# Performance work log

Measured on AMD Instinct MI355X. Metric: run time of the kernel, lower is better.

Reference implementation:

```python
import jax, jax.numpy as jnp
import numpy as np

N_NODES = 100000
N_EDGES = 1600000
N_FEAT = 128
N_CLASSES = 10
N_GRAPHS = 256


def setup_inputs() -> dict:
    key = jax.random.key(0)
    ks = jax.random.split(key, 16)
    x = jax.random.normal(ks[0], (N_NODES, N_FEAT), dtype=jnp.float32)
    edge_index = jax.random.randint(ks[1], (2, N_EDGES), 0, N_NODES, dtype=jnp.int64)
    batch = jnp.sort(jax.random.randint(ks[2], (N_NODES,), 0, N_GRAPHS, dtype=jnp.int64))
    s = 0.1
    # GAT1: in=128 -> heads=8, out_per_head=8, concat -> 64
    W1 = jax.random.normal(ks[3], (N_FEAT, 64), dtype=jnp.float32) * s
    a_src1 = jax.random.normal(ks[4], (8, 8), dtype=jnp.float32) * s
    a_dst1 = jax.random.normal(ks[5], (8, 8), dtype=jnp.float32) * s
    b1 = jnp.zeros((64,), jnp.float32)
    # GAT2: in=64 -> heads=1, out=128
    W2 = jax.random.normal(ks[6], (64, 128), dtype=jnp.float32) * s
    a_src2 = jax.random.normal(ks[7], (1, 128), dtype=jnp.float32) * s
    a_dst2 = jax.random.normal(ks[8], (1, 128), dtype=jnp.float32) * s
    b2 = jnp.zeros((128,), jnp.float32)
    fc_w = jax.random.normal(ks[9], (128, N_CLASSES), dtype=jnp.float32) * s
    fc_b = jnp.zeros((N_CLASSES,), jnp.float32)
    return {"x": x, "edge_index": edge_index, "batch": batch,
            "W1": W1, "a_src1": a_src1, "a_dst1": a_dst1, "b1": b1,
            "W2": W2, "a_src2": a_src2, "a_dst2": a_dst2, "b2": b2,
            "fc_w": fc_w, "fc_b": fc_b}


def _segment_softmax(e, seg, n):
    # e: [E, H]; softmax over edges sharing the same destination node
    m = jax.ops.segment_max(e, seg, num_segments=n)
    m = jnp.where(jnp.isfinite(m), m, jnp.zeros_like(m))  # guard isolated nodes
    ex = jnp.exp(e - m[seg])
    s = jax.ops.segment_sum(ex, seg, num_segments=n)
    return ex / (s[seg] + jnp.asarray(1e-16, e.dtype))


def _gat_conv(x, src, dst, W, a_src, a_dst, bias):
    # PyG GATConv (eval mode, self-loops already appended to src/dst)
    H, C = a_src.shape
    n = x.shape[0]
    h = (x @ W).reshape(n, H, C)                      # [N,H,C]
    al_s = jnp.einsum('nhc,hc->nh', h, a_src)          # [N,H]
    al_d = jnp.einsum('nhc,hc->nh', h, a_dst)
    e = jax.nn.leaky_relu(al_s[src] + al_d[dst], 0.2)  # [E,H]
    alpha = _segment_softmax(e, dst, n)                # [E,H]
    out = jax.ops.segment_sum(h[src] * alpha[..., None], dst, num_segments=n)  # [N,H,C]
    return out.reshape(n, H * C) + bias                # concat=True (H=1 layer2 is identity reshape)


def reference(x, edge_index, batch, W1, a_src1, a_dst1, b1, W2, a_src2, a_dst2, b2, fc_w, fc_b):
    n = x.shape[0]
    loop = jnp.arange(n, dtype=edge_index.dtype)
    src = jnp.concatenate([edge_index[0], loop])       # add self-loops (PyG default)
    dst = jnp.concatenate([edge_index[1], loop])
    x1 = jax.nn.relu(_gat_conv(x, src, dst, W1, a_src1, a_dst1, b1))
    # dropout p=0.6 is identity in eval mode
    x2 = _gat_conv(x1, src, dst, W2, a_src2, a_dst2, b2)
    cnt = jax.ops.segment_sum(jnp.ones((n,), x2.dtype), batch, num_segments=N_GRAPHS)
    pooled = jax.ops.segment_sum(x2, batch, num_segments=N_GRAPHS) / jnp.maximum(cnt, 1.0)[:, None]
    logits = pooled @ fc_w + fc_b
    return jax.nn.log_softmax(logits, axis=1)
```

## Files before the change

### kernel.cpp

```cpp
#include <hip/hip_runtime.h>
#include <math.h>

typedef unsigned int uint;
typedef unsigned short ushort;
typedef unsigned char uchar;
typedef __attribute__((ext_vector_type(2))) float v2f;

#define S1 4.0f
#define S2 16.0f

template <bool HI>
__device__ inline v2f fp8x2f(uint u) {
    return __builtin_amdgcn_cvt_pk_f32_fp8((int)u, HI);
}

__global__ __launch_bounds__(256) void k_gemm1(const float* __restrict__ x,
                                               const float* __restrict__ W1,
                                               const float* __restrict__ as1,
                                               const float* __restrict__ ad1,
                                               uchar* __restrict__ h1f8,
                                               float* __restrict__ al1s,
                                               float* __restrict__ al1d, int N) {
    __shared__ float sB[128 * 64];
    __shared__ float sA[64 * 68];
    const int t = threadIdx.x;
    const int n0 = blockIdx.x * 64;
    {
        const float4* w4 = (const float4*)W1;
        float4* s4 = (float4*)sB;
#pragma unroll
        for (int i = 0; i < 8; ++i) s4[t + i * 256] = w4[t + i * 256];
    }
    const int r0 = (t >> 3) * 2;
    const int c0 = (t & 7) * 8;
    float acc0[8] = {0, 0, 0, 0, 0, 0, 0, 0};
    float acc1[8] = {0, 0, 0, 0, 0, 0, 0, 0};
    for (int kb = 0; kb < 2; ++kb) {
        __syncthreads();
#pragma unroll
        for (int i = 0; i < 4; ++i) {
            int idx = t + i * 256;
            int r = idx >> 4, kc = idx & 15;
            int n = n0 + r;
            float4 v = make_float4(0.f, 0.f, 0.f, 0.f);
            if (n < N) v = ((const float4*)x)[(size_t)n * 32 + kb * 16 + kc];
            *(float4*)&sA[r * 68 + kc * 4] = v;
        }
        __syncthreads();
        const float* bptr = &sB[kb * 64 * 64];
#pragma unroll 8
        for (int kk = 0; kk < 64; ++kk) {
            float a0 = sA[r0 * 68 + kk];
            float a1 = sA[(r0 + 1) * 68 + kk];
            const float* bp = &bptr[kk * 64 + c0];
            float4 b0 = *(const float4*)bp;
            float4 b1v = *(const float4*)(bp + 4);
            acc0[0] += a0 * b0.x; acc0[1] += a0 * b0.y; acc0[2] += a0 * b0.z; acc0[3] += a0 * b0.w;
            acc0[4] += a0 * b1v.x; acc0[5] += a0 * b1v.y; acc0[6] += a0 * b1v.z; acc0[7] += a0 * b1v.w;
            acc1[0] += a1 * b0.x; acc1[1] += a1 * b0.y; acc1[2] += a1 * b0.z; acc1[3] += a1 * b0.w;
            acc1[4] += a1 * b1v.x; acc1[5] += a1 * b1v.y; acc1[6] += a1 * b1v.z; acc1[7] += a1 * b1v.w;
        }
    }
    float ps0 = 0.f, pd0 = 0.f, ps1 = 0.f, pd1 = 0.f;
#pragma unroll
    for (int i = 0; i < 8; ++i) {
        float ws = as1[c0 + i], wd = ad1[c0 + i];
        ps0 += acc0[i] * ws; pd0 += acc0[i] * wd;
        ps1 += acc1[i] * ws; pd1 += acc1[i] * wd;
    }
    int n = n0 + r0;
    int head = t & 7;
    if (n < N) {
        int q0 = 0, q1 = 0;
        q0 = __builtin_amdgcn_cvt_pk_fp8_f32(acc0[0] * S1, acc0[1] * S1, q0, false);
        q0 = __builtin_amdgcn_cvt_pk_fp8_f32(acc0[2] * S1, acc0[3] * S1, q0, true);
        q1 = __builtin_amdgcn_cvt_pk_fp8_f32(acc0[4] * S1, acc0[5] * S1, q1, false);
        q1 = __builtin_amdgcn_cvt_pk_fp8_f32(acc0[6] * S1, acc0[7] * S1, q1, true);
        uint2 p; p.x = (uint)q0; p.y = (uint)q1;
        *(uint2*)&h1f8[(size_t)n * 64 + c0] = p;
        al1s[(size_t)n * 8 + head] = ps0;
        al1d[(size_t)n * 8 + head] = pd0;
    }
    if (n + 1 < N) {
        int q0 = 0, q1 = 0;
        q0 = __builtin_amdgcn_cvt_pk_fp8_f32(acc1[0] * S1, acc1[1] * S1, q0, false);
        q0 = __builtin_amdgcn_cvt_pk_fp8_f32(acc1[2] * S1, acc1[3] * S1, q0, true);
        q1 = __builtin_amdgcn_cvt_pk_fp8_f32(acc1[4] * S1, acc1[5] * S1, q1, false);
        q1 = __builtin_amdgcn_cvt_pk_fp8_f32(acc1[6] * S1, acc1[7] * S1, q1, true);
        uint2 p; p.x = (uint)q0; p.y = (uint)q1;
        *(uint2*)&h1f8[(size_t)(n + 1) * 64 + c0] = p;
        al1s[(size_t)(n + 1) * 8 + head] = ps1;
        al1d[(size_t)(n + 1) * 8 + head] = pd1;
    }
}

__global__ __launch_bounds__(256) void k_gemm2(const float* __restrict__ x1pre,
                                               const float* __restrict__ W2,
                                               const float* __restrict__ b1,
                                               const float* __restrict__ as2,
                                               const float* __restrict__ ad2,
                                               uchar* __restrict__ h2f8,
                                               float* __restrict__ al2s,
                                               float* __restrict__ al2d, int N) {
    __shared__ float sB[64 * 128];
    __shared__ float sA[64 * 68];
    const int t = threadIdx.x;
    const int n0 = blockIdx.x * 64;
    {
        const float4* w4 = (const float4*)W2;
        float4* s4 = (float4*)sB;
#pragma unroll
        for (int i = 0; i < 8; ++i) s4[t + i * 256] = w4[t + i * 256];
    }
#pragma unroll
    for (int i = 0; i < 4; ++i) {
        int idx = t + i * 256;
        int r = idx >> 4, kc = idx & 15;
        int n = n0 + r;
        float4 v = make_float4(0.f, 0.f, 0.f, 0.f);
        if (n < N) {
            v = ((const float4*)x1pre)[(size_t)n * 16 + kc];
            float4 bb = ((const float4*)b1)[kc];
            v.x = fmaxf(v.x + bb.x, 0.f);
            v.y = fmaxf(v.y + bb.y, 0.f);
            v.z = fmaxf(v.z + bb.z, 0.f);
            v.w = fmaxf(v.w + bb.w, 0.f);
        }
        *(float4*)&sA[r * 68 + kc * 4] = v;
    }
    __syncthreads();
    const int r0 = (t >> 3) * 2;
    const int cb = (t & 7) * 4;
    float acc0[16], acc1[16];
#pragma unroll
    for (int i = 0; i < 16; ++i) { acc0[i] = 0.f; acc1[i] = 0.f; }
#pragma unroll 4
    for (int k = 0; k < 64; ++k) {
        float a0 = sA[r0 * 68 + k];
        float a1 = sA[(r0 + 1) * 68 + k];
#pragma unroll
        for (int j = 0; j < 4; ++j) {
            float4 b = *(const float4*)&sB[k * 128 + cb + 32 * j];
            acc0[j * 4 + 0] += a0 * b.x; acc0[j * 4 + 1] += a0 * b.y;
            acc0[j * 4 + 2] += a0 * b.z; acc0[j * 4 + 3] += a0 * b.w;
            acc1[j * 4 + 0] += a1 * b.x; acc1[j * 4 + 1] += a1 * b.y;
            acc1[j * 4 + 2] += a1 * b.z; acc1[j * 4 + 3] += a1 * b.w;
        }
    }
    float ps0 = 0.f, pd0 = 0.f, ps1 = 0.f, pd1 = 0.f;
#pragma unroll
    for (int j = 0; j < 4; ++j)
#pragma unroll
        for (int i = 0; i < 4; ++i) {
            int cc = cb + 32 * j + i;
            float ws = as2[cc], wd = ad2[cc];
            ps0 += acc0[j * 4 + i] * ws; pd0 += acc0[j * 4 + i] * wd;
            ps1 += acc1[j * 4 + i] * ws; pd1 += acc1[j * 4 + i] * wd;
        }
#pragma unroll
    for (int off = 1; off < 8; off <<= 1) {
        ps0 += __shfl_xor(ps0, off); pd0 += __shfl_xor(pd0, off);
        ps1 += __shfl_xor(ps1, off); pd1 += __shfl_xor(pd1, off);
    }
    int n = n0 + r0;
    if (n < N) {
#pragma unroll
        for (int j = 0; j < 4; ++j) {
            int q = 0;
            q = __builtin_amdgcn_cvt_pk_fp8_f32(acc0[j * 4 + 0] * S2, acc0[j * 4 + 1] * S2, q, false);
            q = __builtin_amdgcn_cvt_pk_fp8_f32(acc0[j * 4 + 2] * S2, acc0[j * 4 + 3] * S2, q, true);
            *(uint*)&h2f8[(size_t)n * 128 + cb + 32 * j] = (uint)q;
        }
        if ((t & 7) == 0) { al2s[n] = ps0; al2d[n] = pd0; }
    }
    if (n + 1 < N) {
#pragma unroll
        for (int j = 0; j < 4; ++j) {
            int q = 0;
            q = __builtin_amdgcn_cvt_pk_fp8_f32(acc1[j * 4 + 0] * S2, acc1[j * 4 + 1] * S2, q, false);
            q = __builtin_amdgcn_cvt_pk_fp8_f32(acc1[j * 4 + 2] * S2, acc1[j * 4 + 3] * S2, q, true);
            *(uint*)&h2f8[(size_t)(n + 1) * 128 + cb + 32 * j] = (uint)q;
        }
        if ((t & 7) == 0) { al2s[n + 1] = ps1; al2d[n + 1] = pd1; }
    }
}


__global__ __launch_bounds__(256) void k_hist(const int* __restrict__ dst,
                                              int* __restrict__ counts,
                                              int E, int CH, int NB) {
    __shared__ int hist[784];
    int t = threadIdx.x, b = blockIdx.x;
    for (int k = t; k < NB; k += 256) hist[k] = 0;
    __syncthreads();
    int e0 = b * CH;
    int e1 = e0 + CH; if (e1 > E) e1 = E;
    for (int e = e0 + t; e < e1; e += 256)
        atomicAdd(&hist[dst[e] >> 7], 1);
    __syncthreads();
    for (int k = t; k < NB; k += 256) counts[(size_t)b * NB + k] = hist[k];
}

__global__ __launch_bounds__(256) void k_bscan(int* __restrict__ counts,
                                               int* __restrict__ btot,
                                               int C, int NB) {
    __shared__ int sh[256];
    int t = threadIdx.x, k = blockIdx.x;
    int v[4];
#pragma unroll
    for (int i = 0; i < 4; ++i) {
        int b = t * 4 + i;
        v[i] = (b < C) ? counts[(size_t)b * NB + k] : 0;
    }
    int s = v[0] + v[1] + v[2] + v[3];
    sh[t] = s;
    __syncthreads();
    int accv = s;
    for (int off = 1; off < 256; off <<= 1) {
        int u = (t >= off) ? sh[t - off] : 0;
        __syncthreads();
        accv += u;
        sh[t] = accv;
        __syncthreads();
    }
    int excl = accv - s;
#pragma unroll
    for (int i = 0; i < 4; ++i) {
        int b = t * 4 + i;
        if (b < C) counts[(size_t)b * NB + k] = excl;
        excl += v[i];
    }
    if (t == 255) btot[k] = accv;
}

__global__ void k_bscan2(const int* __restrict__ btot, int* __restrict__ bbase,
                         int NB, int E) {
    __shared__ int sh[1024];
    int t = threadIdx.x;
    int v = (t < NB) ? btot[t] : 0;
    sh[t] = v;
    __syncthreads();
    int accv = v;
    for (int off = 1; off < 1024; off <<= 1) {
        int u = (t >= off) ? sh[t - off] : 0;
        __syncthreads();
        accv += u;
        sh[t] = accv;
        __syncthreads();
    }
    if (t < NB) bbase[t] = accv - v;
    if (t == 0) bbase[NB] = E;
}

__global__ __launch_bounds__(256) void k_bucket(const int* __restrict__ src,
                                                const int* __restrict__ dst,
                                                const int* __restrict__ counts,
                                                const int* __restrict__ bbase,
                                                int2* __restrict__ ebuf,
                                                int E, int CH, int NB) {
    __shared__ int pos[784];
    int t = threadIdx.x, b = blockIdx.x;
    for (int k = t; k < NB; k += 256)
        pos[k] = bbase[k] + counts[(size_t)b * NB + k];
    __syncthreads();
    int e0 = b * CH;
    int e1 = e0 + CH; if (e1 > E) e1 = E;
    for (int e = e0 + t; e < e1; e += 256) {
        int d = dst[e], s = src[e];
        int p = atomicAdd(&pos[d >> 7], 1);
        ebuf[p] = make_int2(s, d);
    }
}

__global__ __launch_bounds__(256) void k_csr(const int* __restrict__ bbase,
                                             const int2* __restrict__ ebuf,
                                             int* __restrict__ row_ptr,
                                             int* __restrict__ col,
                                             int N, int E) {
    __shared__ int cnt[128];
    __shared__ int fill[128];
    __shared__ int rowb[128];
    __shared__ int sh[256];
    int t = threadIdx.x, k = blockIdx.x;
    int lo = bbase[k], hi = bbase[k + 1];
    int nlo = k << 7;
    int nn = N - nlo; if (nn > 128) nn = 128;
    if (t < 128) { cnt[t] = 0; fill[t] = 0; }
    __syncthreads();
    for (int i = lo + t; i < hi; i += 256)
        atomicAdd(&cnt[ebuf[i].y & 127], 1);
    __syncthreads();
    int v = (t < nn) ? (cnt[t] + 1) : 0;
    sh[t] = v;
    __syncthreads();
    int accv = v;
    for (int off = 1; off < 256; off <<= 1) {
        int u = (t >= off) ? sh[t - off] : 0;
        __syncthreads();
        accv += u;
        sh[t] = accv;
        __syncthreads();
    }
    int fbase = lo + nlo;
    if (t < nn) {
        int rb = fbase + accv - v;
        rowb[t] = rb;
        row_ptr[nlo + t] = rb;
        col[rb + cnt[t]] = nlo + t;
    }
    if (k == 0 && t == 0) row_ptr[N] = E + N;
    __syncthreads();
    for (int i = lo + t; i < hi; i += 256) {
        int2 e = ebuf[i];
        int j = e.y & 127;
        int r = atomicAdd(&fill[j], 1);
        col[rowb[j] + r] = e.x;
    }
}

__global__ __launch_bounds__(256) void k_edge1(const uchar* __restrict__ h1f8,
                                               const float* __restrict__ al1s,
                                               const float* __restrict__ al1d,
                                               const int* __restrict__ row_ptr,
                                               const int* __restrict__ col,
                                               float* __restrict__ x1pre, int N) {
    int node = blockIdx.x * 4 + (threadIdx.x >> 6);
    if (node >= N) return;
    const int lane = threadIdx.x & 63;
    const int e8 = lane >> 3;
    const int h = lane & 7;
    const int g = lane >> 4;
    const int k4 = lane & 15;
    const int hh = k4 >> 1;
    float a_d = al1d[(size_t)node * 8 + h];
    const int s0 = row_ptr[node], s1 = row_ptr[node + 1];
    float den_part = 0.f;
    float acc[4] = {0.f, 0.f, 0.f, 0.f};
    for (int base = s0; base < s1; base += 64) {
        int idx = base + lane;
        int cidx = idx < s1 ? idx : s1 - 1;
        int my_col = col[cidx];
        int cnt = s1 - base; if (cnt > 64) cnt = 64;
        int cntR = (cnt + 7) & ~7;
        int i = 0;
        for (; i + 16 <= cntR; i += 16) {
            int cA = __shfl(my_col, i + g);
            int cB = __shfl(my_col, i + 4 + g);
            int cC = __shfl(my_col, i + 8 + g);
            int cD = __shfl(my_col, i + 12 + g);
            uint hA = *(const uint*)(h1f8 + (size_t)cA * 64 + k4 * 4);
            uint hB = *(const uint*)(h1f8 + (size_t)cB * 64 + k4 * 4);
            uint hC = *(const uint*)(h1f8 + (size_t)cC * 64 + k4 * 4);
            uint hD = *(const uint*)(h1f8 + (size_t)cD * 64 + k4 * 4);
            int c0 = __shfl(my_col, i + e8);
            int c1 = __shfl(my_col, i + 8 + e8);
            float e0v = al1s[(size_t)c0 * 8 + h] + a_d;
            float e1v = al1s[(size_t)c1 * 8 + h] + a_d;
            e0v = e0v > 0.f ? e0v : 0.2f * e0v;
            e1v = e1v > 0.f ? e1v : 0.2f * e1v;
            float w0 = (base + i + e8 < s1) ? __expf(e0v) : 0.f;
            float w1 = (base + i + 8 + e8 < s1) ? __expf(e1v) : 0.f;
            den_part += w0 + w1;
            float wA = __shfl(w0, g * 8 + hh);
            float wB = __shfl(w0, (4 + g) * 8 + hh);
            float wC = __shfl(w1, g * 8 + hh);
            float wD = __shfl(w1, (4 + g) * 8 + hh);
            v2f p;
            p = fp8x2f<false>(hA); acc[0] += wA * p.x; acc[1] += wA * p.y;
            p = fp8x2f<true>(hA);  acc[2] += wA * p.x; acc[3] += wA * p.y;
            p = fp8x2f<false>(hB); acc[0] += wB * p.x; acc[1] += wB * p.y;
            p = fp8x2f<true>(hB);  acc[2] += wB * p.x; acc[3] += wB * p.y;
            p = fp8x2f<false>(hC); acc[0] += wC * p.x; acc[1] += wC * p.y;
            p = fp8x2f<true>(hC);  acc[2] += wC * p.x; acc[3] += wC * p.y;
            p = fp8x2f<false>(hD); acc[0] += wD * p.x; acc[1] += wD * p.y;
            p = fp8x2f<true>(hD);  acc[2] += wD * p.x; acc[3] += wD * p.y;
        }
        if (i < cntR) {
            int cA = __shfl(my_col, i + g);
            int cB = __shfl(my_col, i + 4 + g);
            uint hA = *(const uint*)(h1f8 + (size_t)cA * 64 + k4 * 4);
            uint hB = *(const uint*)(h1f8 + (size_t)cB * 64 + k4 * 4);
            int c0 = __shfl(my_col, i + e8);
            float e0v = al1s[(size_t)c0 * 8 + h] + a_d;
            e0v = e0v > 0.f ? e0v : 0.2f * e0v;
            float w0 = (base + i + e8 < s1) ? __expf(e0v) : 0.f;
            den_part += w0;
            float wA = __shfl(w0, g * 8 + hh);
            float wB = __shfl(w0, (4 + g) * 8 + hh);
            v2f p;
            p = fp8x2f<false>(hA); acc[0] += wA * p.x; acc[1] += wA * p.y;
            p = fp8x2f<true>(hA);  acc[2] += wA * p.x; acc[3] += wA * p.y;
            p = fp8x2f<false>(hB); acc[0] += wB * p.x; acc[1] += wB * p.y;
            p = fp8x2f<true>(hB);  acc[2] += wB * p.x; acc[3] += wB * p.y;
        }
    }
#pragma unroll
    for (int i = 0; i < 4; ++i) {
        acc[i] += __shfl_xor(acc[i], 16);
        acc[i] += __shfl_xor(acc[i], 32);
    }
    den_part += __shfl_xor(den_part, 8);
    den_part += __shfl_xor(den_part, 16);
    den_part += __shfl_xor(den_part, 32);
    float den = __shfl(den_part, hh);
    if (lane < 16) {
        float invd = 1.f / (den * S1);
        ((float4*)x1pre)[(size_t)node * 16 + k4] =
            make_float4(acc[0] * invd, acc[1] * invd, acc[2] * invd, acc[3] * invd);
    }
}

__global__ __launch_bounds__(256) void k_edge2(const uchar* __restrict__ h2f8,
                                               const float* __restrict__ al2s,
                                               const float* __restrict__ al2d,
                                               const int* __restrict__ row_ptr,
                                               const int* __restrict__ col,
                                               const float* __restrict__ b2,
                                               float* __restrict__ x2, int N) {
    int node = blockIdx.x * 4 + (threadIdx.x >> 6);
    if (node >= N) return;
    const int lane = threadIdx.x & 63;
    const int g = lane >> 4;
    const int k8 = lane & 15;
    float a_d = al2d[node];
    int s0 = row_ptr[node], s1 = row_ptr[node + 1];
    float acc[8];
#pragma unroll
    for (int i = 0; i < 8; ++i) acc[i] = 0.f;
    float den = 0.f;
    for (int base = s0; base < s1; base += 64) {
        int idx = base + lane;
        int cidx = idx < s1 ? idx : s1 - 1;
        int my_col = col[cidx];
        float my_e = al2s[my_col] + a_d;
        my_e = my_e > 0.f ? my_e : 0.2f * my_e;
        float my_w = (idx < s1) ? __expf(my_e) : 0.f;
        den += my_w;
        int cnt = s1 - base; if (cnt > 64) cnt = 64;
        int cntR = (cnt + 7) & ~7;
        int i = 0;
        for (; i + 16 <= cntR; i += 16) {
            int eA = i + g, eB = i + 4 + g, eC = i + 8 + g, eD = i + 12 + g;
            int cA = __shfl(my_col, eA), cB = __shfl(my_col, eB);
            int cC = __shfl(my_col, eC), cD = __shfl(my_col, eD);
            float wA = __shfl(my_w, eA), wB = __shfl(my_w, eB);
            float wC = __shfl(my_w, eC), wD = __shfl(my_w, eD);
            uint2 hA = *(const uint2*)(h2f8 + (size_t)cA * 128 + k8 * 8);
            uint2 hB = *(const uint2*)(h2f8 + (size_t)cB * 128 + k8 * 8);
            uint2 hC = *(const uint2*)(h2f8 + (size_t)cC * 128 + k8 * 8);
            uint2 hD = *(const uint2*)(h2f8 + (size_t)cD * 128 + k8 * 8);
            v2f p;
            p = fp8x2f<false>(hA.x); acc[0] += wA * p.x; acc[1] += wA * p.y;
            p = fp8x2f<true>(hA.x);  acc[2] += wA * p.x; acc[3] += wA * p.y;
            p = fp8x2f<false>(hA.y); acc[4] += wA * p.x; acc[5] += wA * p.y;
            p = fp8x2f<true>(hA.y);  acc[6] += wA * p.x; acc[7] += wA * p.y;
            p = fp8x2f<false>(hB.x); acc[0] += wB * p.x; acc[1] += wB * p.y;
            p = fp8x2f<true>(hB.x);  acc[2] += wB * p.x; acc[3] += wB * p.y;
            p = fp8x2f<false>(hB.y); acc[4] += wB * p.x; acc[5] += wB * p.y;
            p = fp8x2f<true>(hB.y);  acc[6] += wB * p.x; acc[7] += wB * p.y;
            p = fp8x2f<false>(hC.x); acc[0] += wC * p.x; acc[1] += wC * p.y;
            p = fp8x2f<true>(hC.x);  acc[2] += wC * p.x; acc[3] += wC * p.y;
            p = fp8x2f<false>(hC.y); acc[4] += wC * p.x; acc[5] += wC * p.y;
            p = fp8x2f<true>(hC.y);  acc[6] += wC * p.x; acc[7] += wC * p.y;
            p = fp8x2f<false>(hD.x); acc[0] += wD * p.x; acc[1] += wD * p.y;
            p = fp8x2f<true>(hD.x);  acc[2] += wD * p.x; acc[3] += wD * p.y;
            p = fp8x2f<false>(hD.y); acc[4] += wD * p.x; acc[5] += wD * p.y;
            p = fp8x2f<true>(hD.y);  acc[6] += wD * p.x; acc[7] += wD * p.y;
        }
        if (i < cntR) {
            int eA = i + g, eB = i + 4 + g;
            int cA = __shfl(my_col, eA), cB = __shfl(my_col, eB);
            float wA = __shfl(my_w, eA), wB = __shfl(my_w, eB);
            uint2 hA = *(const uint2*)(h2f8 + (size_t)cA * 128 + k8 * 8);
            uint2 hB = *(const uint2*)(h2f8 + (size_t)cB * 128 + k8 * 8);
            v2f p;
            p = fp8x2f<false>(hA.x); acc[0] += wA * p.x; acc[1] += wA * p.y;
            p = fp8x2f<true>(hA.x);  acc[2] += wA * p.x; acc[3] += wA * p.y;
            p = fp8x2f<false>(hA.y); acc[4] += wA * p.x; acc[5] += wA * p.y;
            p = fp8x2f<true>(hA.y);  acc[6] += wA * p.x; acc[7] += wA * p.y;
            p = fp8x2f<false>(hB.x); acc[0] += wB * p.x; acc[1] += wB * p.y;
            p = fp8x2f<true>(hB.x);  acc[2] += wB * p.x; acc[3] += wB * p.y;
            p = fp8x2f<false>(hB.y); acc[4] += wB * p.x; acc[5] += wB * p.y;
            p = fp8x2f<true>(hB.y);  acc[6] += wB * p.x; acc[7] += wB * p.y;
        }
    }
#pragma unroll
    for (int off = 1; off < 64; off <<= 1) den += __shfl_xor(den, off);
#pragma unroll
    for (int i = 0; i < 8; ++i) {
        acc[i] += __shfl_xor(acc[i], 16);
        acc[i] += __shfl_xor(acc[i], 32);
    }
    if (lane < 16) {
        float invd = 1.f / (den * S2);
        const float4* bb = (const float4*)b2;
        float4 o0 = bb[k8 * 2], o1 = bb[k8 * 2 + 1];
        float4* dst = (float4*)(x2 + (size_t)node * 128 + k8 * 8);
        dst[0] = make_float4(acc[0] * invd + o0.x, acc[1] * invd + o0.y,
                             acc[2] * invd + o0.z, acc[3] * invd + o0.w);
        dst[1] = make_float4(acc[4] * invd + o1.x, acc[5] * invd + o1.y,
                             acc[6] * invd + o1.z, acc[7] * invd + o1.w);
    }
}

__global__ __launch_bounds__(128) void k_pool(const float* __restrict__ x2,
                                              const int* __restrict__ batch,
                                              float* __restrict__ pooled,
                                              float* __restrict__ cnt, int N) {
    int t = threadIdx.x;
    int nstart = blockIdx.x * 128;
    if (nstart >= N) return;
    int nend = nstart + 128;
    if (nend > N) nend = N;
    float acc = 0.f;
    int cur = batch[nstart];
    int count = 0;
    for (int n = nstart; n < nend; ++n) {
        int g = batch[n];
        if (g != cur) {
            atomicAdd(&pooled[(size_t)cur * 128 + t], acc);
            if (t == 0) atomicAdd(&cnt[cur], (float)count);
            acc = 0.f;
            count = 0;
            cur = g;
        }
        acc += x2[(size_t)n * 128 + t];
        ++count;
    }
    atomicAdd(&pooled[(size_t)cur * 128 + t], acc);
    if (t == 0) atomicAdd(&cnt[cur], (float)count);
}

__global__ __launch_bounds__(64) void k_fc(const float* __restrict__ pooled,
                                           const float* __restrict__ cnt,
                                           const float* __restrict__ fcw,
                                           const float* __restrict__ fcb,
                                           float* __restrict__ out, int G) {
    int g = blockIdx.x;
    int c = threadIdx.x;
    float2 p = ((const float2*)pooled)[(size_t)g * 64 + c];
    float inv = 1.f / fmaxf(cnt[g], 1.f);
    p.x *= inv; p.y *= inv;
    float l[10];
#pragma unroll
    for (int j = 0; j < 10; ++j)
        l[j] = p.x * fcw[(2 * c) * 10 + j] + p.y * fcw[(2 * c + 1) * 10 + j];
#pragma unroll
    for (int j = 0; j < 10; ++j)
        for (int off = 1; off < 64; off <<= 1) l[j] += __shfl_xor(l[j], off);
    if (c == 0) {
        float lj[10];
        float m = -1e30f;
#pragma unroll
        for (int j = 0; j < 10; ++j) {
            lj[j] = l[j] + fcb[j];
            m = fmaxf(m, lj[j]);
        }
        float s = 0.f;
#pragma unroll
        for (int j = 0; j < 10; ++j) s += expf(lj[j] - m);
        float ls = logf(s);
#pragma unroll
        for (int j = 0; j < 10; ++j) out[(size_t)g * 10 + j] = lj[j] - m - ls;
    }
}

extern "C" void kernel_launch(void* const* d_in, const int* in_sizes, int n_in,
                              void* d_out, int out_size, void* d_ws, size_t ws_size,
                              hipStream_t stream) {
    const float* x     = (const float*)d_in[0];
    const int*   ei    = (const int*)d_in[1];
    const int*   batch = (const int*)d_in[2];
    const float* W1    = (const float*)d_in[3];
    const float* as1   = (const float*)d_in[4];
    const float* ad1   = (const float*)d_in[5];
    const float* b1    = (const float*)d_in[6];
    const float* W2    = (const float*)d_in[7];
    const float* as2   = (const float*)d_in[8];
    const float* ad2   = (const float*)d_in[9];
    const float* b2    = (const float*)d_in[10];
    const float* fcw   = (const float*)d_in[11];
    const float* fcb   = (const float*)d_in[12];
    float* out = (float*)d_out;

    const int N = in_sizes[0] / 128;
    const int E = in_sizes[1] / 2;
    const int G = out_size / 10;
    const int* srcp = ei;
    const int* dstp = ei + E;

    float* wf = (float*)d_ws;
    uchar* h1f8   = (uchar*)wf;
    float* x1pre  = wf + (size_t)N * 16;
    float* x2     = wf;
    uchar* h2f8   = (uchar*)(wf + (size_t)N * 128);
    float* al1s_  = wf + (size_t)N * 160;
    float* al1d_  = wf + (size_t)N * 168;
    float* al2s_  = wf + (size_t)N * 176;
    float* al2d_  = wf + (size_t)N * 177;
    float* pooled = wf + (size_t)N * 178;
    float* cnt    = pooled + (size_t)G * 128;

    const int NB = (N + 127) >> 7;
    const int C  = 1024;
    const int CH = (E + C - 1) / C;

    int* ib = (int*)(((uintptr_t)(cnt + G) + 15) & ~(uintptr_t)15);
    int2* ebuf   = (int2*)ib;
    int* counts  = ib + 2 * (size_t)E;
    int* btot    = counts + (size_t)C * NB;
    int* bbase   = btot + NB;
    int* row_ptr = bbase + NB + 1;
    int* col     = row_ptr + N + 1;

    size_t zbytes = ((size_t)G * 128 + G) * sizeof(float);
    (void)hipMemsetAsync(pooled, 0, zbytes, stream);

    const int nb64 = (N + 63) / 64;
    const int nb4  = (N + 3) / 4;
    const int nbP  = (N + 127) / 128;

    k_hist<<<C, 256, 0, stream>>>(dstp, counts, E, CH, NB);
    k_gemm1<<<nb64, 256, 0, stream>>>(x, W1, as1, ad1, h1f8, al1s_, al1d_, N);
    k_bscan<<<NB, 256, 0, stream>>>(counts, btot, C, NB);
    k_bscan2<<<1, 1024, 0, stream>>>(btot, bbase, NB, E);
    k_bucket<<<C, 256, 0, stream>>>(srcp, dstp, counts, bbase, ebuf, E, CH, NB);
    k_csr<<<NB, 256, 0, stream>>>(bbase, ebuf, row_ptr, col, N, E);
    k_edge1<<<nb4, 256, 0, stream>>>(h1f8, al1s_, al1d_, row_ptr, col, x1pre, N);
    k_gemm2<<<nb64, 256, 0, stream>>>(x1pre, W2, b1, as2, ad2, h2f8, al2s_, al2d_, N);
    k_edge2<<<nb4, 256, 0, stream>>>(h2f8, al2s_, al2d_, row_ptr, col, b2, x2, N);
    k_pool<<<nbP, 128, 0, stream>>>(x2, batch, pooled, cnt, N);
    k_fc<<<G, 64, 0, stream>>>(pooled, cnt, fcw, fcb, out, G);
}
```

Measured before the change: 357.3 us.

## Pack bucketed edges into single int, use packed f32 FMA and finer tail handling

The bucketed edge buffer now stores each edge as one 32-bit word: a 25-bit source id plus the 7-bit local destination. This halves the traffic written by k_bucket and read by k_csr. The edge kernels switch to packed two-wide float accumulators so the compiler can emit packed FMAs, and build addresses with 32-bit shift/or instead of 64-bit multiplies. They also pad the tail to 4 edges instead of 8, with separate 8- and 4-edge remainder blocks, cutting wasted gathers. The packing assumes node ids fit in 25 bits.

New measurement: 360.3 us. No clear change (+0.8%).

```diff
diff --git a/kernel.cpp b/kernel.cpp
--- a/kernel.cpp
+++ b/kernel.cpp
@@ -256,7 +256,7 @@
                                                 const int* __restrict__ dst,
                                                 const int* __restrict__ counts,
                                                 const int* __restrict__ bbase,
-                                                int2* __restrict__ ebuf,
+                                                int* __restrict__ ebuf,
                                                 int E, int CH, int NB) {
     __shared__ int pos[784];
     int t = threadIdx.x, b = blockIdx.x;
@@ -268,12 +268,12 @@
     for (int e = e0 + t; e < e1; e += 256) {
         int d = dst[e], s = src[e];
         int p = atomicAdd(&pos[d >> 7], 1);
-        ebuf[p] = make_int2(s, d);
+        ebuf[p] = (int)((uint)s | ((uint)(d & 127) << 25));
     }
 }
 
 __global__ __launch_bounds__(256) void k_csr(const int* __restrict__ bbase,
-                                             const int2* __restrict__ ebuf,
+                                             const int* __restrict__ ebuf,
                                              int* __restrict__ row_ptr,
                                              int* __restrict__ col,
                                              int N, int E) {
@@ -288,7 +288,7 @@
     if (t < 128) { cnt[t] = 0; fill[t] = 0; }
     __syncthreads();
     for (int i = lo + t; i < hi; i += 256)
-        atomicAdd(&cnt[ebuf[i].y & 127], 1);
+        atomicAdd(&cnt[((uint)ebuf[i]) >> 25], 1);
     __syncthreads();
     int v = (t < nn) ? (cnt[t] + 1) : 0;
     sh[t] = v;
@@ -311,10 +311,10 @@
     if (k == 0 && t == 0) row_ptr[N] = E + N;
     __syncthreads();
     for (int i = lo + t; i < hi; i += 256) {
-        int2 e = ebuf[i];
-        int j = e.y & 127;
+        uint e = (uint)ebuf[i];
+        int j = (int)(e >> 25);
         int r = atomicAdd(&fill[j], 1);
-        col[rowb[j] + r] = e.x;
+        col[rowb[j] + r] = (int)(e & 0x1FFFFFFu);
     }
 }
 
@@ -332,30 +332,32 @@
     const int g = lane >> 4;
     const int k4 = lane & 15;
     const int hh = k4 >> 1;
-    float a_d = al1d[(size_t)node * 8 + h];
+    const uint co = (uint)(k4 * 4);
+    float a_d = al1d[(((uint)node) << 3) | (uint)h];
     const int s0 = row_ptr[node], s1 = row_ptr[node + 1];
     float den_part = 0.f;
-    float acc[4] = {0.f, 0.f, 0.f, 0.f};
+    v2f accL = {0.f, 0.f};
+    v2f accH = {0.f, 0.f};
     for (int base = s0; base < s1; base += 64) {
         int idx = base + lane;
         int cidx = idx < s1 ? idx : s1 - 1;
         int my_col = col[cidx];
         int cnt = s1 - base; if (cnt > 64) cnt = 64;
-        int cntR = (cnt + 7) & ~7;
+        int cntR = (cnt + 3) & ~3;
         int i = 0;
         for (; i + 16 <= cntR; i += 16) {
             int cA = __shfl(my_col, i + g);
             int cB = __shfl(my_col, i + 4 + g);
             int cC = __shfl(my_col, i + 8 + g);
             int cD = __shfl(my_col, i + 12 + g);
-            uint hA = *(const uint*)(h1f8 + (size_t)cA * 64 + k4 * 4);
-            uint hB = *(const uint*)(h1f8 + (size_t)cB * 64 + k4 * 4);
-            uint hC = *(const uint*)(h1f8 + (size_t)cC * 64 + k4 * 4);
-            uint hD = *(const uint*)(h1f8 + (size_t)cD * 64 + k4 * 4);
+            uint hA = *(const uint*)(h1f8 + ((((uint)cA) << 6) | co));
+            uint hB = *(const uint*)(h1f8 + ((((uint)cB) << 6) | co));
+            uint hC = *(const uint*)(h1f8 + ((((uint)cC) << 6) | co));
+            uint hD = *(const uint*)(h1f8 + ((((uint)cD) << 6) | co));
             int c0 = __shfl(my_col, i + e8);
             int c1 = __shfl(my_col, i + 8 + e8);
-            float e0v = al1s[(size_t)c0 * 8 + h] + a_d;
-            float e1v = al1s[(size_t)c1 * 8 + h] + a_d;
+            float e0v = *(al1s + ((((uint)c0) << 3) | (uint)h)) + a_d;
+            float e1v = *(al1s + ((((uint)c1) << 3) | (uint)h)) + a_d;
             e0v = e0v > 0.f ? e0v : 0.2f * e0v;
             e1v = e1v > 0.f ? e1v : 0.2f * e1v;
             float w0 = (base + i + e8 < s1) ? __expf(e0v) : 0.f;
@@ -365,40 +367,55 @@
             float wB = __shfl(w0, (4 + g) * 8 + hh);
             float wC = __shfl(w1, g * 8 + hh);
             float wD = __shfl(w1, (4 + g) * 8 + hh);
-            v2f p;
-            p = fp8x2f<false>(hA); acc[0] += wA * p.x; acc[1] += wA * p.y;
-            p = fp8x2f<true>(hA);  acc[2] += wA * p.x; acc[3] += wA * p.y;
-            p = fp8x2f<false>(hB); acc[0] += wB * p.x; acc[1] += wB * p.y;
-            p = fp8x2f<true>(hB);  acc[2] += wB * p.x; acc[3] += wB * p.y;
-            p = fp8x2f<false>(hC); acc[0] += wC * p.x; acc[1] += wC * p.y;
-            p = fp8x2f<true>(hC);  acc[2] += wC * p.x; acc[3] += wC * p.y;
-            p = fp8x2f<false>(hD); acc[0] += wD * p.x; acc[1] += wD * p.y;
-            p = fp8x2f<true>(hD);  acc[2] += wD * p.x; acc[3] += wD * p.y;
-        }
-        if (i < cntR) {
+            v2f wA2 = {wA, wA}, wB2 = {wB, wB}, wC2 = {wC, wC}, wD2 = {wD, wD};
+            accL += wA2 * fp8x2f<false>(hA);
+            accH += wA2 * fp8x2f<true>(hA);
+            accL += wB2 * fp8x2f<false>(hB);
+            accH += wB2 * fp8x2f<true>(hB);
+            accL += wC2 * fp8x2f<false>(hC);
+            accH += wC2 * fp8x2f<true>(hC);
+            accL += wD2 * fp8x2f<false>(hD);
+            accH += wD2 * fp8x2f<true>(hD);
+        }
+        int rem = cntR - i;
+        if (rem & 8) {
             int cA = __shfl(my_col, i + g);
             int cB = __shfl(my_col, i + 4 + g);
-            uint hA = *(const uint*)(h1f8 + (size_t)cA * 64 + k4 * 4);
-            uint hB = *(const uint*)(h1f8 + (size_t)cB * 64 + k4 * 4);
+            uint hA = *(const uint*)(h1f8 + ((((uint)cA) << 6) | co));
+            uint hB = *(const uint*)(h1f8 + ((((uint)cB) << 6) | co));
             int c0 = __shfl(my_col, i + e8);
-            float e0v = al1s[(size_t)c0 * 8 + h] + a_d;
+            float e0v = *(al1s + ((((uint)c0) << 3) | (uint)h)) + a_d;
             e0v = e0v > 0.f ? e0v : 0.2f * e0v;
             float w0 = (base + i + e8 < s1) ? __expf(e0v) : 0.f;
             den_part += w0;
             float wA = __shfl(w0, g * 8 + hh);
             float wB = __shfl(w0, (4 + g) * 8 + hh);
-            v2f p;
-            p = fp8x2f<false>(hA); acc[0] += wA * p.x; acc[1] += wA * p.y;
-            p = fp8x2f<true>(hA);  acc[2] += wA * p.x; acc[3] += wA * p.y;
-            p = fp8x2f<false>(hB); acc[0] += wB * p.x; acc[1] += wB * p.y;
-            p = fp8x2f<true>(hB);  acc[2] += wB * p.x; acc[3] += wB * p.y;
-        }
-    }
-#pragma unroll
-    for (int i = 0; i < 4; ++i) {
-        acc[i] += __shfl_xor(acc[i], 16);
-        acc[i] += __shfl_xor(acc[i], 32);
-    }
+            v2f wA2 = {wA, wA}, wB2 = {wB, wB};
+            accL += wA2 * fp8x2f<false>(hA);
+            accH += wA2 * fp8x2f<true>(hA);
+            accL += wB2 * fp8x2f<false>(hB);
+            accH += wB2 * fp8x2f<true>(hB);
+            i += 8;
+        }
+        if (rem & 4) {
+            int cA = __shfl(my_col, i + g);
+            uint hA = *(const uint*)(h1f8 + ((((uint)cA) << 6) | co));
+            int c0 = __shfl(my_col, i + e8);
+            float e0v = *(al1s + ((((uint)c0) << 3) | (uint)h)) + a_d;
+            e0v = e0v > 0.f ? e0v : 0.2f * e0v;
+            float w0 = (base + i + e8 < s1) ? __expf(e0v) : 0.f;
+            den_part += w0;
+            float wA = __shfl(w0, g * 8 + hh);
+            v2f wA2 = {wA, wA};
+            accL += wA2 * fp8x2f<false>(hA);
+            accH += wA2 * fp8x2f<true>(hA);
+        }
+    }
+    float a0 = accL.x, a1 = accL.y, a2 = accH.x, a3 = accH.y;
+    a0 += __shfl_xor(a0, 16); a0 += __shfl_xor(a0, 32);
+    a1 += __shfl_xor(a1, 16); a1 += __shfl_xor(a1, 32);
+    a2 += __shfl_xor(a2, 16); a2 += __shfl_xor(a2, 32);
+    a3 += __shfl_xor(a3, 16); a3 += __shfl_xor(a3, 32);
     den_part += __shfl_xor(den_part, 8);
     den_part += __shfl_xor(den_part, 16);
     den_part += __shfl_xor(den_part, 32);
@@ -406,7 +423,7 @@
     if (lane < 16) {
         float invd = 1.f / (den * S1);
         ((float4*)x1pre)[(size_t)node * 16 + k4] =
-            make_float4(acc[0] * invd, acc[1] * invd, acc[2] * invd, acc[3] * invd);
+            make_float4(a0 * invd, a1 * invd, a2 * invd, a3 * invd);
     }
 }
 
@@ -422,22 +439,21 @@
     const int lane = threadIdx.x & 63;
     const int g = lane >> 4;
     const int k8 = lane & 15;
+    const uint co = (uint)(k8 * 8);
     float a_d = al2d[node];
     int s0 = row_ptr[node], s1 = row_ptr[node + 1];
-    float acc[8];
-#pragma unroll
-    for (int i = 0; i < 8; ++i) acc[i] = 0.f;
+    v2f acc0 = {0.f, 0.f}, acc1 = {0.f, 0.f}, acc2 = {0.f, 0.f}, acc3 = {0.f, 0.f};
     float den = 0.f;
     for (int base = s0; base < s1; base += 64) {
         int idx = base + lane;
         int cidx = idx < s1 ? idx : s1 - 1;
         int my_col = col[cidx];
-        float my_e = al2s[my_col] + a_d;
+        float my_e = *(al2s + (uint)my_col) + a_d;
         my_e = my_e > 0.f ? my_e : 0.2f * my_e;
         float my_w = (idx < s1) ? __expf(my_e) : 0.f;
         den += my_w;
         int cnt = s1 - base; if (cnt > 64) cnt = 64;
-        int cntR = (cnt + 7) & ~7;
+        int cntR = (cnt + 3) & ~3;
         int i = 0;
         for (; i + 16 <= cntR; i += 16) {
             int eA = i + g, eB = i + 4 + g, eC = i + 8 + g, eD = i + 12 + g;
@@ -445,61 +461,79 @@
             int cC = __shfl(my_col, eC), cD = __shfl(my_col, eD);
             float wA = __shfl(my_w, eA), wB = __shfl(my_w, eB);
             float wC = __shfl(my_w, eC), wD = __shfl(my_w, eD);
-            uint2 hA = *(const uint2*)(h2f8 + (size_t)cA * 128 + k8 * 8);
-            uint2 hB = *(const uint2*)(h2f8 + (size_t)cB * 128 + k8 * 8);
-            uint2 hC = *(const uint2*)(h2f8 + (size_t)cC * 128 + k8 * 8);
-            uint2 hD = *(const uint2*)(h2f8 + (size_t)cD * 128 + k8 * 8);
-            v2f p;
-            p = fp8x2f<false>(hA.x); acc[0] += wA * p.x; acc[1] += wA * p.y;
-            p = fp8x2f<true>(hA.x);  acc[2] += wA * p.x; acc[3] += wA * p.y;
-            p = fp8x2f<false>(hA.y); acc[4] += wA * p.x; acc[5] += wA * p.y;
-            p = fp8x2f<true>(hA.y);  acc[6] += wA * p.x; acc[7] += wA * p.y;
-            p = fp8x2f<false>(hB.x); acc[0] += wB * p.x; acc[1] += wB * p.y;
-            p = fp8x2f<true>(hB.x);  acc[2] += wB * p.x; acc[3] += wB * p.y;
-            p = fp8x2f<false>(hB.y); acc[4] += wB * p.x; acc[5] += wB * p.y;
-            p = fp8x2f<true>(hB.y);  acc[6] += wB * p.x; acc[7] += wB * p.y;
-            p = fp8x2f<false>(hC.x); acc[0] += wC * p.x; acc[1] += wC * p.y;
-            p = fp8x2f<true>(hC.x);  acc[2] += wC * p.x; acc[3] += wC * p.y;
-            p = fp8x2f<false>(hC.y); acc[4] += wC * p.x; acc[5] += wC * p.y;
-            p = fp8x2f<true>(hC.y);  acc[6] += wC * p.x; acc[7] += wC * p.y;
-            p = fp8x2f<false>(hD.x); acc[0] += wD * p.x; acc[1] += wD * p.y;
-            p = fp8x2f<true>(hD.x);  acc[2] += wD * p.x; acc[3] += wD * p.y;
-            p = fp8x2f<false>(hD.y); acc[4] += wD * p.x; acc[5] += wD * p.y;
-            p = fp8x2f<true>(hD.y);  acc[6] += wD * p.x; acc[7] += wD * p.y;
-        }
-        if (i < cntR) {
+            uint2 hA = *(const uint2*)(h2f8 + ((((uint)cA) << 7) | co));
+            uint2 hB = *(const uint2*)(h2f8 + ((((uint)cB) << 7) | co));
+            uint2 hC = *(const uint2*)(h2f8 + ((((uint)cC) << 7) | co));
+            uint2 hD = *(const uint2*)(h2f8 + ((((uint)cD) << 7) | co));
+            v2f wA2 = {wA, wA}, wB2 = {wB, wB}, wC2 = {wC, wC}, wD2 = {wD, wD};
+            acc0 += wA2 * fp8x2f<false>(hA.x);
+            acc1 += wA2 * fp8x2f<true>(hA.x);
+            acc2 += wA2 * fp8x2f<false>(hA.y);
+            acc3 += wA2 * fp8x2f<true>(hA.y);
+            acc0 += wB2 * fp8x2f<false>(hB.x);
+            acc1 += wB2 * fp8x2f<true>(hB.x);
+            acc2 += wB2 * fp8x2f<false>(hB.y);
+            acc3 += wB2 * fp8x2f<true>(hB.y);
+            acc0 += wC2 * fp8x2f<false>(hC.x);
+            acc1 += wC2 * fp8x2f<true>(hC.x);
+            acc2 += wC2 * fp8x2f<false>(hC.y);
+            acc3 += wC2 * fp8x2f<true>(hC.y);
+            acc0 += wD2 * fp8x2f<false>(hD.x);
+            acc1 += wD2 * fp8x2f<true>(hD.x);
+            acc2 += wD2 * fp8x2f<false>(hD.y);
+            acc3 += wD2 * fp8x2f<true>(hD.y);
+        }
+        int rem = cntR - i;
+        if (rem & 8) {
             int eA = i + g, eB = i + 4 + g;
             int cA = __shfl(my_col, eA), cB = __shfl(my_col, eB);
             float wA = __shfl(my_w, eA), wB = __shfl(my_w, eB);
-            uint2 hA = *(const uint2*)(h2f8 + (size_t)cA * 128 + k8 * 8);
-            uint2 hB = *(const uint2*)(h2f8 + (size_t)cB * 128 + k8 * 8);
-            v2f p;
-            p = fp8x2f<false>(hA.x); acc[0] += wA * p.x; acc[1] += wA * p.y;
-            p = fp8x2f<true>(hA.x);  acc[2] += wA * p.x; acc[3] += wA * p.y;
-            p = fp8x2f<false>(hA.y); acc[4] += wA * p.x; acc[5] += wA * p.y;
-            p = fp8x2f<true>(hA.y);  acc[6] += wA * p.x; acc[7] += wA * p.y;
-            p = fp8x2f<false>(hB.x); acc[0] += wB * p.x; acc[1] += wB * p.y;
-            p = fp8x2f<true>(hB.x);  acc[2] += wB * p.x; acc[3] += wB * p.y;
-            p = fp8x2f<false>(hB.y); acc[4] += wB * p.x; acc[5] += wB * p.y;
-            p = fp8x2f<true>(hB.y);  acc[6] += wB * p.x; acc[7] += wB * p.y;
+            uint2 hA = *(const uint2*)(h2f8 + ((((uint)cA) << 7) | co));
+            uint2 hB = *(const uint2*)(h2f8 + ((((uint)cB) << 7) | co));
+            v2f wA2 = {wA, wA}, wB2 = {wB, wB};
+            acc0 += wA2 * fp8x2f<false>(hA.x);
+            acc1 += wA2 * fp8x2f<true>(hA.x);
+            acc2 += wA2 * fp8x2f<false>(hA.y);
+            acc3 += wA2 * fp8x2f<true>(hA.y);
+            acc0 += wB2 * fp8x2f<false>(hB.x);
+            acc1 += wB2 * fp8x2f<true>(hB.x);
+            acc2 += wB2 * fp8x2f<false>(hB.y);
+            acc3 += wB2 * fp8x2f<true>(hB.y);
+            i += 8;
+        }
+        if (rem & 4) {
+            int eA = i + g;
+            int cA = __shfl(my_col, eA);
+            float wA = __shfl(my_w, eA);
+            uint2 hA = *(const uint2*)(h2f8 + ((((uint)cA) << 7) | co));
+            v2f wA2 = {wA, wA};
+            acc0 += wA2 * fp8x2f<false>(hA.x);
+            acc1 += wA2 * fp8x2f<true>(hA.x);
+            acc2 += wA2 * fp8x2f<false>(hA.y);
+            acc3 += wA2 * fp8x2f<true>(hA.y);
         }
     }
 #pragma unroll
     for (int off = 1; off < 64; off <<= 1) den += __shfl_xor(den, off);
-#pragma unroll
-    for (int i = 0; i < 8; ++i) {
-        acc[i] += __shfl_xor(acc[i], 16);
-        acc[i] += __shfl_xor(acc[i], 32);
-    }
+    float r0 = acc0.x, r1 = acc0.y, r2 = acc1.x, r3 = acc1.y;
+    float r4 = acc2.x, r5 = acc2.y, r6 = acc3.x, r7 = acc3.y;
+    r0 += __shfl_xor(r0, 16); r0 += __shfl_xor(r0, 32);
+    r1 += __shfl_xor(r1, 16); r1 += __shfl_xor(r1, 32);
+    r2 += __shfl_xor(r2, 16); r2 += __shfl_xor(r2, 32);
+    r3 += __shfl_xor(r3, 16); r3 += __shfl_xor(r3, 32);
+    r4 += __shfl_xor(r4, 16); r4 += __shfl_xor(r4, 32);
+    r5 += __shfl_xor(r5, 16); r5 += __shfl_xor(r5, 32);
+    r6 += __shfl_xor(r6, 16); r6 += __shfl_xor(r6, 32);
+    r7 += __shfl_xor(r7, 16); r7 += __shfl_xor(r7, 32);
     if (lane < 16) {
         float invd = 1.f / (den * S2);
         const float4* bb = (const float4*)b2;
         float4 o0 = bb[k8 * 2], o1 = bb[k8 * 2 + 1];
         float4* dst = (float4*)(x2 + (size_t)node * 128 + k8 * 8);
-        dst[0] = make_float4(acc[0] * invd + o0.x, acc[1] * invd + o0.y,
-                             acc[2] * invd + o0.z, acc[3] * invd + o0.w);
-        dst[1] = make_float4(acc[4] * invd + o1.x, acc[5] * invd + o1.y,
-                             acc[6] * invd + o1.z, acc[7] * invd + o1.w);
+        dst[0] = make_float4(r0 * invd + o0.x, r1 * invd + o0.y,
+                             r2 * invd + o0.z, r3 * invd + o0.w);
+        dst[1] = make_float4(r4 * invd + o1.x, r5 * invd + o1.y,
+                             r6 * invd + o1.z, r7 * invd + o1.w);
     }
 }
 
@@ -606,8 +640,8 @@
     const int CH = (E + C - 1) / C;
 
     int* ib = (int*)(((uintptr_t)(cnt + G) + 15) & ~(uintptr_t)15);
-    int2* ebuf   = (int2*)ib;
-    int* counts  = ib + 2 * (size_t)E;
+    int* ebuf    = ib;
+    int* counts  = ib + (size_t)E;
     int* btot    = counts + (size_t)C * NB;
     int* bbase   = btot + NB;
     int* row_ptr = bbase + NB + 1;
```
